# Kernel tuning notes

Hardware: AMD Instinct MI355X
Metric: run time of the kernel (lower is better)

The kernel has to match this reference:

```python
import jax, jax.numpy as jnp
import numpy as np
from jax import lax

B, T, C, H, W = 2, 64, 32, 64, 64   # (batch, feat-channels t, bands c, height, width)
NH = 4                              # num_heads; head dim = C//NH
HID = int(T * 2.66)                 # GDFN hidden channels = 170
EPS_LN = 1e-5
EPS_L2 = 1e-12


def _dwconv3d(x, w, pad):
    # x: (B, Cg, D, H, W); w: (Cg, 1, kd, kh, kw) depthwise
    cg = x.shape[1]
    return lax.conv_general_dilated(
        x, w, window_strides=(1, 1, 1), padding=pad,
        dimension_numbers=('NCDHW', 'OIDHW', 'NCDHW'),
        feature_group_count=cg)


def _pw(w, x):
    # 1x1x1 conv == channel GEMM; w: (out, in)
    return jnp.einsum('oi,bidhw->bodhw', w, x)


def _ln_ch(x, g, b):
    # LayerNorm over channel dim (dim1), matching reshape/transpose dance in torch
    m = jnp.mean(x, axis=1, keepdims=True)
    v = jnp.var(x, axis=1, keepdims=True)
    xn = (x - m) * lax.rsqrt(v + EPS_LN)
    return xn * g[None, :, None, None, None] + b[None, :, None, None, None]


def _attn(x, temperature, qkv_w, qkv_dw, attn_out_w):
    b, t, c, h, w = x.shape
    qkv = _dwconv3d(_pw(qkv_w, x), qkv_dw, ((0, 0), (1, 1), (1, 1)))  # (b,3t,c,h,w)
    q, k, v = jnp.split(qkv, 3, axis=1)
    L = h * w * t
    X = (t * c * h * w) // (NH * L)  # == c // NH
    rsh = lambda a: a.reshape(b, NH, X, L)
    q, k, v = rsh(q), rsh(k), rsh(v)
    l2n = lambda a: a / jnp.maximum(jnp.linalg.norm(a, axis=-1, keepdims=True), EPS_L2)
    q, k = l2n(q), l2n(k)
    scores = jnp.einsum('bnxl,bnyl->bnxy', q, k) * temperature  # (b,NH,X,X)
    att = jax.nn.softmax(scores, axis=-1)
    o = jnp.einsum('bnxy,bnyl->bnxl', att, v).reshape(b, t, c, h, w)
    return _pw(attn_out_w, o)


def _ffn(x, pin_w, dw_w, pout_w):
    y = _dwconv3d(_pw(pin_w, x), dw_w, ((1, 1), (1, 1), (1, 1)))  # (b,2*HID,c,h,w)
    x1, x2 = jnp.split(y, 2, axis=1)
    return _pw(pout_w, jax.nn.gelu(x1, approximate=False) * x2)


def setup_inputs() -> dict:
    key = jax.random.key(0)
    ks = jax.random.split(key, 12)
    s = lambda *sh: 1.0 / np.sqrt(np.prod(sh[1:]) if len(sh) > 1 else 1.0)
    p = lambda k, *sh: jax.random.normal(k, sh, dtype=jnp.float32) * s(*sh)
    return {
        'x': jax.random.normal(ks[0], (B, T, C, H, W), dtype=jnp.float32),
        'norm1_g': jnp.ones((T,), jnp.float32),
        'norm1_b': jnp.zeros((T,), jnp.float32),
        'temperature': jnp.ones((1, NH, 1, 1), jnp.float32),
        'qkv_w': p(ks[1], 3 * T, T),
        'qkv_dw': p(ks[2], 3 * T, 1, 1, 3, 3),
        'attn_out_w': p(ks[3], T, T),
        'norm2_g': jnp.ones((T,), jnp.float32),
        'norm2_b': jnp.zeros((T,), jnp.float32),
        'pin_w': p(ks[4], 2 * HID, T),
        'dw_w': p(ks[5], 2 * HID, 1, 3, 3, 3),
        'pout_w': p(ks[6], T, HID),
        'se_w': p(ks[7], T, T),
        'se_b': jnp.zeros((T,), jnp.float32),
    }


def reference(x, norm1_g, norm1_b, temperature, qkv_w, qkv_dw, attn_out_w,
              norm2_g, norm2_b, pin_w, dw_w, pout_w, se_w, se_b):
    x = x + _attn(_ln_ch(x, norm1_g, norm1_b), temperature, qkv_w, qkv_dw, attn_out_w)
    x = x + _ffn(_ln_ch(x, norm2_g, norm2_b), pin_w, dw_w, pout_w)
    s = jnp.mean(x, axis=(2, 3, 4), keepdims=True)               # GlobalAvgPool3d
    s = jax.nn.sigmoid(_pw(se_w, s) + se_b[None, :, None, None, None])
    return s * x
```

## Files before the change

### kernel.cpp

```cpp
#include <hip/hip_runtime.h>
#include <hip/hip_bf16.h>
#include <math.h>

typedef __hip_bfloat16 bf16;

#define S_ 131072

#define OFF_QKVW 0
#define OFF_AOW  12288
#define OFF_PINW 16384
#define OFF_POUTW 38912
#define OFF_SEW  49792
#define OFF_QDW  53888
#define OFF_DWW  55616
#define OFF_N1G  64796
#define OFF_N1B  64860
#define OFF_N2G  64924
#define OFF_N2B  64988
#define OFF_SEB  65052
#define OFF_TEMP 65116
#define WB_TOTAL 65120

#define SM_SSQ 0
#define SM_SSK 64
#define SM_ATT 128
#define SM_MEAN 640
#define SM_SVEC 768
#define SM_M 896
#define SM_FLAGI 9216

#define WSOFF_SM 262144
#define WSOFF_X1 303104
#define WSOFF_R  33857536
#define WS_REQUIRED 134520832ull

#define NCHUNK 256
#define PROW 44

__device__ __forceinline__ float toF(float v) { return v; }
__device__ __forceinline__ float toF(bf16 v) { return __bfloat162float(v); }

__device__ __forceinline__ float bfbitsToF(unsigned short u) {
  union { unsigned int i; float f; } x;
  x.i = ((unsigned int)u) << 16;
  return x.f;
}

__device__ __forceinline__ unsigned short bfBits(float f) {
  bf16 h = __float2bfloat16(f);
  return *reinterpret_cast<unsigned short*>(&h);
}

__device__ __forceinline__ float ldIn(const void* p, size_t i, int isbf) {
  return isbf ? __bfloat162float(((const bf16*)p)[i]) : ((const float*)p)[i];
}
__device__ __forceinline__ void stOut(void* p, size_t i, int isbf, float v) {
  if (isbf) ((bf16*)p)[i] = __float2bfloat16(v);
  else ((float*)p)[i] = v;
}

__device__ __forceinline__ float wred(float v) {
#pragma unroll
  for (int o = 32; o > 0; o >>= 1) v += __shfl_down(v, o, 64);
  return v;
}

__device__ __forceinline__ void conv4(const bf16* __restrict__ plane,
                                      const float* __restrict__ w9,
                                      int h, int w0, bool wlo, bool whi,
                                      float& o0, float& o1, float& o2, float& o3) {
  o0 = o1 = o2 = o3 = 0.f;
#pragma unroll
  for (int rr = 0; rr < 3; ++rr) {
    int hh = h - 1 + rr;
    if ((unsigned)hh < 64u) {
      const bf16* row = plane + hh * 64 + w0;
      ushort4 m = *reinterpret_cast<const ushort4*>(row);
      float v1 = bfbitsToF(m.x), v2 = bfbitsToF(m.y);
      float v3 = bfbitsToF(m.z), v4 = bfbitsToF(m.w);
      float v0 = wlo ? toF(row[-1]) : 0.f;
      float v5 = whi ? toF(row[4]) : 0.f;
      float wa = w9[rr * 3 + 0], wbb = w9[rr * 3 + 1], wc = w9[rr * 3 + 2];
      o0 = fmaf(wa, v0, fmaf(wbb, v1, fmaf(wc, v2, o0)));
      o1 = fmaf(wa, v1, fmaf(wbb, v2, fmaf(wc, v3, o1)));
      o2 = fmaf(wa, v2, fmaf(wbb, v3, fmaf(wc, v4, o2)));
      o3 = fmaf(wa, v3, fmaf(wbb, v4, fmaf(wc, v5, o3)));
    }
  }
}

__global__ void zero_sm(float* sm, const unsigned* n1g_raw) {
  for (int i = threadIdx.x; i < 768; i += 256) sm[i] = 0.f;
  if (threadIdx.x == 0) {
    ((int*)sm)[SM_FLAGI] = ((n1g_raw[0] & 0xFFFFu) != 0u) ? 1 : 0;
  }
}

__global__ void convert_w(const void* qkvw, const void* aow, const void* pinw,
                          const void* poutw, const void* sew, const void* qdw,
                          const void* dww, const void* n1g, const void* n1b,
                          const void* n2g, const void* n2b, const void* seb,
                          const void* temp, float* wb, const int* dflag) {
  int i = blockIdx.x * 256 + threadIdx.x;
  if (i >= WB_TOTAL) return;
  int f = *dflag;
  float v;
  if (i < OFF_AOW) v = ldIn(qkvw, i, f);
  else if (i < OFF_PINW) v = ldIn(aow, i - OFF_AOW, f);
  else if (i < OFF_POUTW) { int r = i - OFF_PINW; v = (r < 21760) ? ldIn(pinw, r, f) : 0.f; }
  else if (i < OFF_SEW) v = ldIn(poutw, i - OFF_POUTW, f);
  else if (i < OFF_QDW) v = ldIn(sew, i - OFF_SEW, f);
  else if (i < OFF_DWW) v = ldIn(qdw, i - OFF_QDW, f);
  else if (i < OFF_N1G) v = ldIn(dww, i - OFF_DWW, f);
  else if (i < OFF_N1B) v = ldIn(n1g, i - OFF_N1G, f);
  else if (i < OFF_N2G) v = ldIn(n1b, i - OFF_N1B, f);
  else if (i < OFF_N2B) v = ldIn(n2g, i - OFF_N2G, f);
  else if (i < OFF_SEB) v = ldIn(n2b, i - OFF_N2B, f);
  else if (i < OFF_TEMP) v = ldIn(seb, i - OFF_SEB, f);
  else v = ldIn(temp, i - OFF_TEMP, f);
  wb[i] = v;
}

__global__ __launch_bounds__(256) void qkv_ln_gemm(const void* __restrict__ x,
                                                   const float* __restrict__ wb,
                                                   bf16* __restrict__ qraw,
                                                   const int* __restrict__ dflag) {
  __shared__ bf16 tile[64][256];
  int tid = threadIdx.x;
  int p0 = blockIdx.x << 8;
  int b = p0 >> 17, s0 = p0 & (S_ - 1);
  int isbf = *dflag;
  float xin[64];
  if (isbf) {
    const bf16* src = (const bf16*)x + (size_t)b * 64 * S_ + s0;
#pragma unroll
    for (int i = 0; i < 8; ++i) {
      int q = i * 256 + tid;
      int row = q >> 5;
      int col8 = (q & 31) * 8;
      *reinterpret_cast<uint4*>(&tile[row][col8]) =
          *reinterpret_cast<const uint4*>(src + (size_t)row * S_ + col8);
    }
    __syncthreads();
#pragma unroll
    for (int t = 0; t < 64; ++t) xin[t] = toF(tile[t][tid]);
  } else {
    const float* xf = (const float*)x + (size_t)b * 64 * S_ + s0 + tid;
#pragma unroll
    for (int t = 0; t < 64; ++t) xin[t] = xf[(size_t)t * S_];
  }
  float sum = 0.f;
#pragma unroll
  for (int t = 0; t < 64; ++t) sum += xin[t];
  float mean = sum * (1.f / 64.f);
  float ss = 0.f;
#pragma unroll
  for (int t = 0; t < 64; ++t) { float d = xin[t] - mean; ss += d * d; }
  float rstd = rsqrtf(ss * (1.f / 64.f) + 1e-5f);
#pragma unroll
  for (int t = 0; t < 64; ++t)
    xin[t] = (xin[t] - mean) * rstd * wb[OFF_N1G + t] + wb[OFF_N1B + t];
  size_t obase = (size_t)b * 192 * S_ + s0 + tid;
  for (int oc = 0; oc < 192; oc += 16) {
    float acc[16];
#pragma unroll
    for (int j = 0; j < 16; ++j) acc[j] = 0.f;
    const float* wp = wb + OFF_QKVW + oc * 64;
#pragma unroll
    for (int t = 0; t < 64; ++t) {
      float xv = xin[t];
#pragma unroll
      for (int j = 0; j < 16; ++j) acc[j] = fmaf(wp[j * 64 + t], xv, acc[j]);
    }
#pragma unroll
    for (int j = 0; j < 16; ++j)
      qraw[obase + (size_t)(oc + j) * S_] = __float2bfloat16(acc[j]);
  }
}

__global__ __launch_bounds__(256, 4) void attn_scores(const bf16* __restrict__ qraw,
                                                      const float* __restrict__ wb,
                                                      float* __restrict__ part) {
  int blk = blockIdx.x;
  int bh = blk >> 9, qh = (blk >> 8) & 1, chunk = blk & (NCHUNK - 1);
  int b = bh >> 2, nh = bh & 3;
  int pbit = chunk >> 7;
  int c = (chunk >> 2) & 31;
  int hq = chunk & 3;
  int tid = threadIdx.x;
  int wseg = tid & 15, w0 = wseg * 4;
  int h = hq * 16 + (tid >> 4);
  bool wlo = (wseg != 0), whi = (wseg != 15);

  float dq[4], dk[8], dot[32], qv[4][4];
#pragma unroll
  for (int i = 0; i < 4; ++i) dq[i] = 0.f;
#pragma unroll
  for (int i = 0; i < 8; ++i) dk[i] = 0.f;
#pragma unroll
  for (int i = 0; i < 32; ++i) dot[i] = 0.f;

  const size_t bbase = ((size_t)(b * 192)) << 17;

#pragma unroll
  for (int r = 0; r < 4; ++r) {
    int ch = 2 * (nh * 8 + qh * 4 + r) + pbit;
    const bf16* pl = qraw + bbase + (((size_t)ch) << 17) + (c << 12);
    float o0, o1, o2, o3;
    conv4(pl, wb + OFF_QDW + ch * 9, h, w0, wlo, whi, o0, o1, o2, o3);
    qv[r][0] = o0; qv[r][1] = o1; qv[r][2] = o2; qv[r][3] = o3;
    dq[r] = fmaf(o0, o0, fmaf(o1, o1, fmaf(o2, o2, fmaf(o3, o3, dq[r]))));
  }
#pragma unroll
  for (int r = 0; r < 8; ++r) {
    int ch = 64 + 2 * (nh * 8 + r) + pbit;
    const bf16* pl = qraw + bbase + (((size_t)ch) << 17) + (c << 12);
    float k0, k1, k2, k3;
    conv4(pl, wb + OFF_QDW + ch * 9, h, w0, wlo, whi, k0, k1, k2, k3);
    dk[r] = fmaf(k0, k0, fmaf(k1, k1, fmaf(k2, k2, fmaf(k3, k3, dk[r]))));
#pragma unroll
    for (int i = 0; i < 4; ++i)
      dot[i * 8 + r] = fmaf(qv[i][0], k0, fmaf(qv[i][1], k1,
                       fmaf(qv[i][2], k2, fmaf(qv[i][3], k3, dot[i * 8 + r]))));
  }

  __shared__ float red[4][PROW];
  int lane = threadIdx.x & 63, wid = threadIdx.x >> 6;
#pragma unroll
  for (int i = 0; i < 4; ++i) {
    float v = wred(dq[i]);
    if (lane == 0) red[wid][i] = v;
  }
#pragma unroll
  for (int i = 0; i < 8; ++i) {
    float v = wred(dk[i]);
    if (lane == 0) red[wid][4 + i] = v;
  }
#pragma unroll
  for (int ij = 0; ij < 32; ++ij) {
    float v = wred(dot[ij]);
    if (lane == 0) red[wid][12 + ij] = v;
  }
  __syncthreads();
  if (threadIdx.x < PROW)
    part[blk * PROW + threadIdx.x] = red[0][threadIdx.x] + red[1][threadIdx.x] +
                                     red[2][threadIdx.x] + red[3][threadIdx.x];
}

__global__ void attn_reduce(const float* __restrict__ part, float* __restrict__ sm) {
  int o = blockIdx.x;
  int bh = o / 80, v = o - bh * 80;
  int qi, off;
  if (v < 8) {
    qi = v >> 2; off = v & 3;
  } else if (v < 16) {
    qi = 0; off = 4 + (v - 8);
  } else {
    int idx = v - 16;
    int i = idx >> 3, j = idx & 7;
    qi = i >> 2; off = 12 + (i & 3) * 8 + j;
  }
  __shared__ float s[256];
  s[threadIdx.x] = part[(((size_t)bh * 2 + qi) * NCHUNK + threadIdx.x) * PROW + off];
  __syncthreads();
#pragma unroll
  for (int st = 128; st > 0; st >>= 1) {
    if (threadIdx.x < st) s[threadIdx.x] += s[threadIdx.x + st];
    __syncthreads();
  }
  if (threadIdx.x == 0) {
    float r = s[0];
    if (v < 8) sm[SM_SSQ + bh * 8 + v] = r;
    else if (v < 16) sm[SM_SSK + bh * 8 + (v - 8)] = r;
    else sm[SM_ATT + bh * 64 + (v - 16)] = r;
  }
}

__global__ __launch_bounds__(256) void v_dwconv(const bf16* __restrict__ qraw,
                                                const float* __restrict__ wb,
                                                bf16* __restrict__ vc) {
  int blk = blockIdx.x;
  int hq = blk & 3, c = (blk >> 2) & 31, tv = (blk >> 7) & 63, b = blk >> 13;
  int tid = threadIdx.x;
  int wseg = tid & 15, w0 = wseg * 4;
  int h = hq * 16 + (tid >> 4);
  bool wlo = (wseg != 0), whi = (wseg != 15);
  const bf16* pl = qraw + (((size_t)(b * 192 + 128 + tv)) << 17) + (c << 12);
  float o0, o1, o2, o3;
  conv4(pl, wb + OFF_QDW + (128 + tv) * 9, h, w0, wlo, whi, o0, o1, o2, o3);
  bf16* dst = vc + (((size_t)(b * 64 + tv)) << 17) + (c << 12) + h * 64 + w0;
  ushort4 st;
  st.x = bfBits(o0); st.y = bfBits(o1); st.z = bfBits(o2); st.w = bfBits(o3);
  *reinterpret_cast<ushort4*>(dst) = st;
}

__global__ void attn_softmax_m(float* __restrict__ sm, const float* __restrict__ wb) {
  int t = threadIdx.x;
  if (t < 64) {
    int bh = t >> 3, i = t & 7, nh = bh & 3;
    float invq = 1.f / fmaxf(sqrtf(sm[SM_SSQ + bh * 8 + i]), 1e-12f);
    float temp = wb[OFF_TEMP + nh];
    float sc[8];
#pragma unroll
    for (int j = 0; j < 8; ++j) {
      float invk = 1.f / fmaxf(sqrtf(sm[SM_SSK + bh * 8 + j]), 1e-12f);
      sc[j] = sm[SM_ATT + bh * 64 + i * 8 + j] * invq * invk * temp;
    }
    float mx = sc[0];
#pragma unroll
    for (int j = 1; j < 8; ++j) mx = fmaxf(mx, sc[j]);
    float sum = 0.f;
#pragma unroll
    for (int j = 0; j < 8; ++j) { sc[j] = expf(sc[j] - mx); sum += sc[j]; }
    float inv = 1.f / sum;
#pragma unroll
    for (int j = 0; j < 8; ++j) sm[SM_ATT + bh * 64 + i * 8 + j] = sc[j] * inv;
  }
  __syncthreads();
  for (int k = 0; k < 32; ++k) {
    int idx = t + k * 256;
    int b = idx >> 12;
    int rest = idx & 4095;
    int tout = rest >> 6, tv = rest & 63;
    int n = (tv >> 4) & 3, j = (tv >> 1) & 7, pbit = tv & 1;
    float acc = 0.f;
#pragma unroll
    for (int i = 0; i < 8; ++i)
      acc = fmaf(wb[OFF_AOW + tout * 64 + ((n * 8 + i) * 2 + pbit)],
                 sm[SM_ATT + (b * 4 + n) * 64 + i * 8 + j], acc);
    sm[SM_M + b * 4096 + tv * 64 + tout] = acc;
  }
}

__global__ __launch_bounds__(256) void attn_apply_gemm(const bf16* __restrict__ vc,
                                                       const float* __restrict__ sm,
                                                       const void* __restrict__ x,
                                                       bf16* __restrict__ x1,
                                                       const int* __restrict__ dflag) {
  __shared__ bf16 tile[64][256];
  int tid = threadIdx.x;
  int p0 = blockIdx.x << 8;
  int b = p0 >> 17, s0 = p0 & (S_ - 1);
  int isbf = *dflag;
  const bf16* src = vc + (((size_t)(b * 64)) << 17) + s0;
#pragma unroll
  for (int i = 0; i < 8; ++i) {
    int q = i * 256 + tid;
    int row = q >> 5;
    int col8 = (q & 31) * 8;
    *reinterpret_cast<uint4*>(&tile[row][col8]) =
        *reinterpret_cast<const uint4*>(src + (size_t)row * S_ + col8);
  }
  __syncthreads();

  const float* Mg = sm + SM_M + b * 4096;
  float acc[64];
#pragma unroll
  for (int j = 0; j < 64; ++j) acc[j] = 0.f;
  for (int t = 0; t < 64; ++t) {
    float v = toF(tile[t][tid]);
    const float* mrow = Mg + t * 64;
#pragma unroll
    for (int j = 0; j < 64; ++j) acc[j] = fmaf(mrow[j], v, acc[j]);
  }

  size_t obase = (size_t)b * 64 * S_ + s0 + tid;
#pragma unroll
  for (int j = 0; j < 64; ++j) {
    size_t oi = obase + (size_t)j * S_;
    x1[oi] = __float2bfloat16(acc[j] + ldIn(x, oi, isbf));
  }
}

__global__ __launch_bounds__(256) void pin_ln_gemm(const bf16* __restrict__ x1,
                                                   const float* __restrict__ wb,
                                                   bf16* __restrict__ slab, int c0) {
  __shared__ bf16 tile[64][256];
  int tid = threadIdx.x;
  int p0 = blockIdx.x << 8;
  int b = p0 >> 17, s0 = p0 & (S_ - 1);
  const bf16* src = x1 + (size_t)b * 64 * S_ + s0;
#pragma unroll
  for (int i = 0; i < 8; ++i) {
    int q = i * 256 + tid;
    int row = q >> 5;
    int col8 = (q & 31) * 8;
    *reinterpret_cast<uint4*>(&tile[row][col8]) =
        *reinterpret_cast<const uint4*>(src + (size_t)row * S_ + col8);
  }
  __syncthreads();

  float xin[64];
  float sum = 0.f;
#pragma unroll
  for (int t = 0; t < 64; ++t) { xin[t] = toF(tile[t][tid]); sum += xin[t]; }
  float mean = sum * (1.f / 64.f);
  float ss = 0.f;
#pragma unroll
  for (int t = 0; t < 64; ++t) { float d = xin[t] - mean; ss += d * d; }
  float rstd = rsqrtf(ss * (1.f / 64.f) + 1e-5f);
#pragma unroll
  for (int t = 0; t < 64; ++t)
    xin[t] = (xin[t] - mean) * rstd * wb[OFF_N2G + t] + wb[OFF_N2B + t];
  int s = s0 + tid;
  size_t obase = (size_t)b * 64 * S_ + s;
  for (int jc = 0; jc < 4; ++jc) {
    float acc[16];
    int rows[16];
#pragma unroll
    for (int jj = 0; jj < 16; ++jj) {
      acc[jj] = 0.f;
      int j = jc * 16 + jj;
      int c1 = c0 + (j & 31);
      rows[jj] = (c1 < 170) ? (c1 + ((j >= 32) ? 170 : 0)) : 0;
    }
#pragma unroll
    for (int t = 0; t < 64; ++t) {
      float xv = xin[t];
#pragma unroll
      for (int jj = 0; jj < 16; ++jj)
        acc[jj] = fmaf(wb[OFF_PINW + rows[jj] * 64 + t], xv, acc[jj]);
    }
#pragma unroll
    for (int jj = 0; jj < 16; ++jj) {
      int j = jc * 16 + jj;
      if (c0 + (j & 31) < 170)
        slab[obase + (size_t)j * S_] = __float2bfloat16(acc[jj]);
    }
  }
}

__global__ __launch_bounds__(256) void dw3d_gelu_chunk(const bf16* __restrict__ slab,
                                                       const float* __restrict__ wb,
                                                       bf16* __restrict__ g,
                                                       int c0, int nch) {
  int blk = blockIdx.x;
  int hq = blk & 3, c = (blk >> 2) & 31;
  int r = blk >> 7;
  int lj = r % nch, b = r / nch;
  int c1 = c0 + lj;
  int tid = threadIdx.x;
  int wseg = tid & 15, w0 = wseg * 4;
  int h = hq * 16 + (tid >> 4);
  bool wlo = (wseg != 0), whi = (wseg != 15);
  const bf16* p1 = slab + (((size_t)(b * 64 + lj)) << 17);
  const bf16* p2 = slab + (((size_t)(b * 64 + 32 + lj)) << 17);
  const float* w1 = wb + OFF_DWW + c1 * 27;
  const float* w2 = wb + OFF_DWW + (c1 + 170) * 27;
  float a10 = 0.f, a11 = 0.f, a12 = 0.f, a13 = 0.f;
  float a20 = 0.f, a21 = 0.f, a22 = 0.f, a23 = 0.f;
#pragma unroll
  for (int dc = -1; dc <= 1; ++dc) {
    int cc = c + dc;
    if ((unsigned)cc >= 32u) continue;
    const bf16* q1 = p1 + ((size_t)cc << 12);
    const bf16* q2 = p2 + ((size_t)cc << 12);
    const float* u1 = w1 + (dc + 1) * 9;
    const float* u2 = w2 + (dc + 1) * 9;
#pragma unroll
    for (int rr = 0; rr < 3; ++rr) {
      int hh = h - 1 + rr;
      if ((unsigned)hh < 64u) {
        const bf16* r1 = q1 + hh * 64 + w0;
        const bf16* r2 = q2 + hh * 64 + w0;
        ushort4 m1 = *reinterpret_cast<const ushort4*>(r1);
        ushort4 m2 = *reinterpret_cast<const ushort4*>(r2);
        float p0 = wlo ? toF(r1[-1]) : 0.f;
        float p5 = whi ? toF(r1[4]) : 0.f;
        float s0 = wlo ? toF(r2[-1]) : 0.f;
        float s5 = whi ? toF(r2[4]) : 0.f;
        float pa = bfbitsToF(m1.x), pb = bfbitsToF(m1.y);
        float pc = bfbitsToF(m1.z), pd = bfbitsToF(m1.w);
        float sa = bfbitsToF(m2.x), sb = bfbitsToF(m2.y);
        float sc = bfbitsToF(m2.z), sd = bfbitsToF(m2.w);
        float wa = u1[rr * 3 + 0], wbv = u1[rr * 3 + 1], wc = u1[rr * 3 + 2];
        a10 = fmaf(wa, p0, fmaf(wbv, pa, fmaf(wc, pb, a10)));
        a11 = fmaf(wa, pa, fmaf(wbv, pb, fmaf(wc, pc, a11)));
        a12 = fmaf(wa, pb, fmaf(wbv, pc, fmaf(wc, pd, a12)));
        a13 = fmaf(wa, pc, fmaf(wbv, pd, fmaf(wc, p5, a13)));
        float xa = u2[rr * 3 + 0], xb = u2[rr * 3 + 1], xc = u2[rr * 3 + 2];
        a20 = fmaf(xa, s0, fmaf(xb, sa, fmaf(xc, sb, a20)));
        a21 = fmaf(xa, sa, fmaf(xb, sb, fmaf(xc, sc, a21)));
        a22 = fmaf(xa, sb, fmaf(xb, sc, fmaf(xc, sd, a22)));
        a23 = fmaf(xa, sc, fmaf(xb, sd, fmaf(xc, s5, a23)));
      }
    }
  }
  float ge0 = 0.5f * a10 * (1.f + erff(a10 * 0.70710678118f));
  float ge1 = 0.5f * a11 * (1.f + erff(a11 * 0.70710678118f));
  float ge2 = 0.5f * a12 * (1.f + erff(a12 * 0.70710678118f));
  float ge3 = 0.5f * a13 * (1.f + erff(a13 * 0.70710678118f));
  int sp = (c << 12) + (h << 6) + w0;
  bf16* dst = g + (((size_t)(b * 170 + c1)) << 17) + sp;
  ushort4 st;
  st.x = bfBits(ge0 * a20); st.y = bfBits(ge1 * a21);
  st.z = bfBits(ge2 * a22); st.w = bfBits(ge3 * a23);
  *reinterpret_cast<ushort4*>(dst) = st;
}

__global__ __launch_bounds__(256, 2) void pout_gemm(const bf16* __restrict__ g,
                                                    const float* __restrict__ wb,
                                                    const bf16* __restrict__ x1,
                                                    void* __restrict__ out,
                                                    float* __restrict__ mean,
                                                    const int* __restrict__ dflag) {
  int blk = blockIdx.x;
  int sblk = blk & 127, jh = (blk >> 7) & 1, b = blk >> 8;
  int s = (sblk << 10) | (threadIdx.x << 2);
  int isbf = *dflag;
  const bf16* ip = g + (size_t)b * 170 * S_ + s;
  const float* wp = wb + OFF_POUTW + (jh * 32) * 170;
  float a0[32], a1[32], a2[32], a3[32];
#pragma unroll
  for (int j = 0; j < 32; ++j) { a0[j] = 0.f; a1[j] = 0.f; a2[j] = 0.f; a3[j] = 0.f; }

  float c0[4], c1[4], c2[4], c3[4];
#pragma unroll
  for (int u = 0; u < 4; ++u) {
    ushort4 m = *reinterpret_cast<const ushort4*>(ip + (size_t)u * S_);
    c0[u] = bfbitsToF(m.x); c1[u] = bfbitsToF(m.y);
    c2[u] = bfbitsToF(m.z); c3[u] = bfbitsToF(m.w);
  }
  for (int t = 0; t < 168; t += 4) {
    float n0[4], n1[4], n2[4], n3[4];
#pragma unroll
    for (int u = 0; u < 4; ++u) {
      ushort4 m = *reinterpret_cast<const ushort4*>(ip + (size_t)(t + 4 + u) * S_);
      n0[u] = bfbitsToF(m.x); n1[u] = bfbitsToF(m.y);
      n2[u] = bfbitsToF(m.z); n3[u] = bfbitsToF(m.w);
    }
#pragma unroll
    for (int u = 0; u < 4; ++u) {
#pragma unroll
      for (int j = 0; j < 32; ++j) {
        float wv = wp[j * 170 + t + u];
        a0[j] = fmaf(wv, c0[u], a0[j]);
        a1[j] = fmaf(wv, c1[u], a1[j]);
        a2[j] = fmaf(wv, c2[u], a2[j]);
        a3[j] = fmaf(wv, c3[u], a3[j]);
      }
    }
#pragma unroll
    for (int u = 0; u < 4; ++u) { c0[u] = n0[u]; c1[u] = n1[u]; c2[u] = n2[u]; c3[u] = n3[u]; }
  }
#pragma unroll
  for (int u = 0; u < 2; ++u) {
#pragma unroll
    for (int j = 0; j < 32; ++j) {
      float wv = wp[j * 170 + 168 + u];
      a0[j] = fmaf(wv, c0[u], a0[j]);
      a1[j] = fmaf(wv, c1[u], a1[j]);
      a2[j] = fmaf(wv, c2[u], a2[j]);
      a3[j] = fmaf(wv, c3[u], a3[j]);
    }
  }

  __shared__ float red[4][32];
  int lane = threadIdx.x & 63, wid = threadIdx.x >> 6;
  size_t obase = (size_t)b * 64 * S_ + s;
#pragma unroll
  for (int j = 0; j < 32; ++j) {
    size_t oi = obase + (size_t)(jh * 32 + j) * S_;
    ushort4 rm = *reinterpret_cast<const ushort4*>(x1 + oi);
    float v0 = a0[j] + bfbitsToF(rm.x);
    float v1 = a1[j] + bfbitsToF(rm.y);
    float v2 = a2[j] + bfbitsToF(rm.z);
    float v3 = a3[j] + bfbitsToF(rm.w);
    stOut(out, oi,     isbf, v0);
    stOut(out, oi + 1, isbf, v1);
    stOut(out, oi + 2, isbf, v2);
    stOut(out, oi + 3, isbf, v3);
    float v = wred(v0 + v1 + v2 + v3);
    if (lane == 0) red[wid][j] = v;
  }
  __syncthreads();
  if (threadIdx.x < 32) {
    float tot = red[0][threadIdx.x] + red[1][threadIdx.x] +
                red[2][threadIdx.x] + red[3][threadIdx.x];
    atomicAdd(&mean[b * 64 + jh * 32 + threadIdx.x], tot * (1.f / S_));
  }
}

__global__ void se_vec(const float* __restrict__ wb, float* __restrict__ sm) {
  int t = threadIdx.x;
  int b = t >> 6, o = t & 63;
  float acc = wb[OFF_SEB + o];
  for (int k = 0; k < 64; ++k)
    acc = fmaf(wb[OFF_SEW + o * 64 + k], sm[SM_MEAN + b * 64 + k], acc);
  sm[SM_SVEC + t] = 1.f / (1.f + expf(-acc));
}

__global__ __launch_bounds__(256) void se_scale(void* __restrict__ xo,
                                                const float* __restrict__ svec,
                                                const int* __restrict__ dflag) {
  size_t i4 = ((size_t)blockIdx.x * 256 + threadIdx.x) * 4;
  int row = (int)(i4 >> 17);
  int isbf = *dflag;
  float sv = svec[row];
  if (isbf) {
    bf16* p = (bf16*)xo + i4;
    ushort4 m = *reinterpret_cast<ushort4*>(p);
    m.x = bfBits(bfbitsToF(m.x) * sv);
    m.y = bfBits(bfbitsToF(m.y) * sv);
    m.z = bfBits(bfbitsToF(m.z) * sv);
    m.w = bfBits(bfbitsToF(m.w) * sv);
    *reinterpret_cast<ushort4*>(p) = m;
  } else {
    float4* p = reinterpret_cast<float4*>((float*)xo + i4);
    float4 m = *p;
    m.x *= sv; m.y *= sv; m.z *= sv; m.w *= sv;
    *p = m;
  }
}

extern "C" void kernel_launch(void* const* d_in, const int* in_sizes, int n_in,
                              void* d_out, int out_size, void* d_ws, size_t ws_size,
                              hipStream_t stream) {
  if (ws_size < WS_REQUIRED) return;

  char* ws = (char*)d_ws;
  float* WB  = (float*)ws;
  float* SM  = (float*)(ws + WSOFF_SM);
  const int* FLAG = (const int*)(SM + SM_FLAGI);
  bf16*  X1  = (bf16*)(ws + WSOFF_X1);
  float* PART= (float*)(ws + WSOFF_X1);
  bf16*  QR  = (bf16*)(ws + WSOFF_R);
  bf16*  G   = (bf16*)(ws + WSOFF_R);
  bf16*  SLAB= (bf16*)d_out;
  bf16*  VC  = (bf16*)d_out;

  zero_sm<<<1, 256, 0, stream>>>(SM, (const unsigned*)d_in[1]);
  convert_w<<<(WB_TOTAL + 255) / 256, 256, 0, stream>>>(
      d_in[4], d_in[6], d_in[9], d_in[11], d_in[12], d_in[5], d_in[10],
      d_in[1], d_in[2], d_in[7], d_in[8], d_in[13], d_in[3], WB, FLAG);

  qkv_ln_gemm<<<1024, 256, 0, stream>>>(d_in[0], WB, QR, FLAG);
  attn_scores<<<8 * 2 * NCHUNK, 256, 0, stream>>>(QR, WB, PART);
  attn_reduce<<<640, 256, 0, stream>>>(PART, SM);
  v_dwconv<<<16384, 256, 0, stream>>>(QR, WB, VC);
  attn_softmax_m<<<1, 256, 0, stream>>>(SM, WB);
  attn_apply_gemm<<<1024, 256, 0, stream>>>(VC, SM, d_in[0], X1, FLAG);

  for (int c0 = 0; c0 < 170; c0 += 32) {
    int nch = (170 - c0 < 32) ? (170 - c0) : 32;
    pin_ln_gemm<<<1024, 256, 0, stream>>>(X1, WB, SLAB, c0);
    dw3d_gelu_chunk<<<nch * 256, 256, 0, stream>>>(SLAB, WB, G, c0, nch);
  }
  pout_gemm<<<512, 256, 0, stream>>>(G, WB, X1, d_out, SM + SM_MEAN, FLAG);

  se_vec<<<1, 128, 0, stream>>>(WB, SM);
  se_scale<<<16384, 256, 0, stream>>>(d_out, SM + SM_SVEC, FLAG);
}
```

Baseline: 1.341 ms.

## Use bf16 MFMA for the QKV pointwise GEMM in the LN+QKV kernel

The bf16 input path of the fused LayerNorm+QKV projection now writes the normalized activations to a transposed LDS tile in bf16. It then computes the 192x64 channel GEMM with 16x16x32 bf16 MFMA instructions, replacing per-thread scalar FMAs. QKV weights are pre-packed into the MFMA fragment layout by the weight conversion kernel into a new workspace region. This cuts VALU work for one of the GEMMs but rounds the normalized activations and weights to bf16 before accumulation, and the output stores are now strided per lane rather than one contiguous element per thread.

```diff
diff --git a/kernel.cpp b/kernel.cpp
--- a/kernel.cpp
+++ b/kernel.cpp
@@ -3,6 +3,8 @@
 #include <math.h>
 
 typedef __hip_bfloat16 bf16;
+typedef __attribute__((ext_vector_type(8))) short bf16x8_t;
+typedef __attribute__((ext_vector_type(4))) float f32x4_t;
 
 #define S_ 131072
 
@@ -20,6 +22,7 @@
 #define OFF_SEB  65052
 #define OFF_TEMP 65116
 #define WB_TOTAL 65120
+#define QPACK_N  12288
 
 #define SM_SSQ 0
 #define SM_SSK 64
@@ -31,6 +34,7 @@
 
 #define WSOFF_SM 262144
 #define WSOFF_X1 303104
+#define WSOFF_QPK (WSOFF_X1 + 1048576)
 #define WSOFF_R  33857536
 #define WS_REQUIRED 134520832ull
 
@@ -100,10 +104,19 @@
                           const void* poutw, const void* sew, const void* qdw,
                           const void* dww, const void* n1g, const void* n1b,
                           const void* n2g, const void* n2b, const void* seb,
-                          const void* temp, float* wb, const int* dflag) {
+                          const void* temp, float* wb, bf16* wpack,
+                          const int* dflag) {
   int i = blockIdx.x * 256 + threadIdx.x;
-  if (i >= WB_TOTAL) return;
+  if (i >= WB_TOTAL + QPACK_N) return;
   int f = *dflag;
+  if (i >= WB_TOTAL) {
+    int p = i - WB_TOTAL;
+    int j = p & 7, lane = (p >> 3) & 63, kt = (p >> 9) & 1, ot = p >> 10;
+    int row = ot * 16 + (lane & 15);
+    int k = kt * 32 + ((lane >> 4) << 3) + j;
+    wpack[p] = __float2bfloat16(ldIn(qkvw, row * 64 + k, f));
+    return;
+  }
   float v;
   if (i < OFF_AOW) v = ldIn(qkvw, i, f);
   else if (i < OFF_PINW) v = ldIn(aow, i - OFF_AOW, f);
@@ -123,14 +136,17 @@
 
 __global__ __launch_bounds__(256) void qkv_ln_gemm(const void* __restrict__ x,
                                                    const float* __restrict__ wb,
+                                                   const bf16* __restrict__ wpack,
                                                    bf16* __restrict__ qraw,
                                                    const int* __restrict__ dflag) {
-  __shared__ bf16 tile[64][256];
+  __shared__ __align__(16) char smem[36864];
+  bf16 (*tile)[256] = reinterpret_cast<bf16(*)[256]>(smem);
+  bf16 (*tileT)[72] = reinterpret_cast<bf16(*)[72]>(smem);
   int tid = threadIdx.x;
   int p0 = blockIdx.x << 8;
   int b = p0 >> 17, s0 = p0 & (S_ - 1);
   int isbf = *dflag;
-  float xin[64];
+
   if (isbf) {
     const bf16* src = (const bf16*)x + (size_t)b * 64 * S_ + s0;
 #pragma unroll
@@ -142,39 +158,88 @@
           *reinterpret_cast<const uint4*>(src + (size_t)row * S_ + col8);
     }
     __syncthreads();
+    float xin[64];
 #pragma unroll
     for (int t = 0; t < 64; ++t) xin[t] = toF(tile[t][tid]);
+    float sum = 0.f;
+#pragma unroll
+    for (int t = 0; t < 64; ++t) sum += xin[t];
+    float mean = sum * (1.f / 64.f);
+    float ss = 0.f;
+#pragma unroll
+    for (int t = 0; t < 64; ++t) { float d = xin[t] - mean; ss += d * d; }
+    float rstd = rsqrtf(ss * (1.f / 64.f) + 1e-5f);
+#pragma unroll
+    for (int t = 0; t < 64; ++t)
+      xin[t] = (xin[t] - mean) * rstd * wb[OFF_N1G + t] + wb[OFF_N1B + t];
+    __syncthreads();
+#pragma unroll
+    for (int q = 0; q < 8; ++q) {
+      uint4 pk;
+      pk.x = (unsigned)bfBits(xin[q * 8 + 0]) | ((unsigned)bfBits(xin[q * 8 + 1]) << 16);
+      pk.y = (unsigned)bfBits(xin[q * 8 + 2]) | ((unsigned)bfBits(xin[q * 8 + 3]) << 16);
+      pk.z = (unsigned)bfBits(xin[q * 8 + 4]) | ((unsigned)bfBits(xin[q * 8 + 5]) << 16);
+      pk.w = (unsigned)bfBits(xin[q * 8 + 6]) | ((unsigned)bfBits(xin[q * 8 + 7]) << 16);
+      *reinterpret_cast<uint4*>(&tileT[tid][q * 8]) = pk;
+    }
+    __syncthreads();
+    int wid = tid >> 6, lane = tid & 63;
+    bf16x8_t bfrag[8];
+#pragma unroll
+    for (int pt = 0; pt < 4; ++pt)
+#pragma unroll
+      for (int kt = 0; kt < 2; ++kt)
+        bfrag[pt * 2 + kt] = *reinterpret_cast<const bf16x8_t*>(
+            &tileT[wid * 64 + pt * 16 + (lane & 15)][kt * 32 + ((lane >> 4) << 3)]);
+    const bf16x8_t* wp8 = reinterpret_cast<const bf16x8_t*>(wpack);
+    size_t obase = (size_t)b * 192 * S_ + s0;
+    for (int ot = 0; ot < 12; ++ot) {
+      bf16x8_t a0 = wp8[(ot * 2 + 0) * 64 + lane];
+      bf16x8_t a1 = wp8[(ot * 2 + 1) * 64 + lane];
+#pragma unroll
+      for (int pt = 0; pt < 4; ++pt) {
+        f32x4_t acc = {0.f, 0.f, 0.f, 0.f};
+        acc = __builtin_amdgcn_mfma_f32_16x16x32_bf16(a0, bfrag[pt * 2 + 0], acc, 0, 0, 0);
+        acc = __builtin_amdgcn_mfma_f32_16x16x32_bf16(a1, bfrag[pt * 2 + 1], acc, 0, 0, 0);
+        int pos = wid * 64 + pt * 16 + (lane & 15);
+        int orow = ot * 16 + ((lane >> 4) << 2);
+#pragma unroll
+        for (int reg = 0; reg < 4; ++reg)
+          qraw[obase + (size_t)(orow + reg) * S_ + pos] = __float2bfloat16(acc[reg]);
+      }
+    }
   } else {
+    float xin[64];
     const float* xf = (const float*)x + (size_t)b * 64 * S_ + s0 + tid;
 #pragma unroll
     for (int t = 0; t < 64; ++t) xin[t] = xf[(size_t)t * S_];
-  }
-  float sum = 0.f;
-#pragma unroll
-  for (int t = 0; t < 64; ++t) sum += xin[t];
-  float mean = sum * (1.f / 64.f);
-  float ss = 0.f;
-#pragma unroll
-  for (int t = 0; t < 64; ++t) { float d = xin[t] - mean; ss += d * d; }
-  float rstd = rsqrtf(ss * (1.f / 64.f) + 1e-5f);
-#pragma unroll
-  for (int t = 0; t < 64; ++t)
-    xin[t] = (xin[t] - mean) * rstd * wb[OFF_N1G + t] + wb[OFF_N1B + t];
-  size_t obase = (size_t)b * 192 * S_ + s0 + tid;
-  for (int oc = 0; oc < 192; oc += 16) {
-    float acc[16];
-#pragma unroll
-    for (int j = 0; j < 16; ++j) acc[j] = 0.f;
-    const float* wp = wb + OFF_QKVW + oc * 64;
-#pragma unroll
-    for (int t = 0; t < 64; ++t) {
-      float xv = xin[t];
-#pragma unroll
-      for (int j = 0; j < 16; ++j) acc[j] = fmaf(wp[j * 64 + t], xv, acc[j]);
-    }
-#pragma unroll
-    for (int j = 0; j < 16; ++j)
-      qraw[obase + (size_t)(oc + j) * S_] = __float2bfloat16(acc[j]);
+    float sum = 0.f;
+#pragma unroll
+    for (int t = 0; t < 64; ++t) sum += xin[t];
+    float mean = sum * (1.f / 64.f);
+    float ss = 0.f;
+#pragma unroll
+    for (int t = 0; t < 64; ++t) { float d = xin[t] - mean; ss += d * d; }
+    float rstd = rsqrtf(ss * (1.f / 64.f) + 1e-5f);
+#pragma unroll
+    for (int t = 0; t < 64; ++t)
+      xin[t] = (xin[t] - mean) * rstd * wb[OFF_N1G + t] + wb[OFF_N1B + t];
+    size_t obase = (size_t)b * 192 * S_ + s0 + tid;
+    for (int oc = 0; oc < 192; oc += 16) {
+      float acc[16];
+#pragma unroll
+      for (int j = 0; j < 16; ++j) acc[j] = 0.f;
+      const float* wp = wb + OFF_QKVW + oc * 64;
+#pragma unroll
+      for (int t = 0; t < 64; ++t) {
+        float xv = xin[t];
+#pragma unroll
+        for (int j = 0; j < 16; ++j) acc[j] = fmaf(wp[j * 64 + t], xv, acc[j]);
+      }
+#pragma unroll
+      for (int j = 0; j < 16; ++j)
+        qraw[obase + (size_t)(oc + j) * S_] = __float2bfloat16(acc[j]);
+    }
   }
 }
 
@@ -624,17 +689,18 @@
   const int* FLAG = (const int*)(SM + SM_FLAGI);
   bf16*  X1  = (bf16*)(ws + WSOFF_X1);
   float* PART= (float*)(ws + WSOFF_X1);
+  bf16*  WPK = (bf16*)(ws + WSOFF_QPK);
   bf16*  QR  = (bf16*)(ws + WSOFF_R);
   bf16*  G   = (bf16*)(ws + WSOFF_R);
   bf16*  SLAB= (bf16*)d_out;
   bf16*  VC  = (bf16*)d_out;
 
   zero_sm<<<1, 256, 0, stream>>>(SM, (const unsigned*)d_in[1]);
-  convert_w<<<(WB_TOTAL + 255) / 256, 256, 0, stream>>>(
+  convert_w<<<(WB_TOTAL + QPACK_N + 255) / 256, 256, 0, stream>>>(
       d_in[4], d_in[6], d_in[9], d_in[11], d_in[12], d_in[5], d_in[10],
-      d_in[1], d_in[2], d_in[7], d_in[8], d_in[13], d_in[3], WB, FLAG);
-
-  qkv_ln_gemm<<<1024, 256, 0, stream>>>(d_in[0], WB, QR, FLAG);
+      d_in[1], d_in[2], d_in[7], d_in[8], d_in[13], d_in[3], WB, WPK, FLAG);
+
+  qkv_ln_gemm<<<1024, 256, 0, stream>>>(d_in[0], WB, WPK, QR, FLAG);
   attn_scores<<<8 * 2 * NCHUNK, 256, 0, stream>>>(QR, WB, PART);
   attn_reduce<<<640, 256, 0, stream>>>(PART, SM);
   v_dwconv<<<16384, 256, 0, stream>>>(QR, WB, VC);
```

After: 1.340 ms. Within noise of the previous version (-0.1%).
